# Kernel tuning notes

Measured on AMD Instinct MI355X. Metric: run time of the kernel, lower is better.

## Reference

```python
import jax, jax.numpy as jnp
import numpy as np

B, S, D, H = 4, 2048, 1024, 16
DK = D // H
EPS = 1e-5


def setup_inputs() -> dict:
    key = jax.random.key(0)
    ks = jax.random.split(key, 9)
    lim = 1.0 / np.sqrt(DK)  # nn.Linear default init range
    def u(k, shape):
        return jax.random.uniform(k, shape, jnp.float32, -lim, lim)
    return {
        "x": jax.random.normal(ks[0], (B, S, D), jnp.float32),
        "Wq": u(ks[1], (H, DK, DK)),
        "bq": u(ks[2], (H, DK)),
        "Wk": u(ks[3], (H, DK, DK)),
        "bk": u(ks[4], (H, DK)),
        "Wv": u(ks[5], (H, DK, DK)),
        "bv": u(ks[6], (H, DK)),
        "gamma": jnp.ones((D,), jnp.float32),
        "beta": jnp.zeros((D,), jnp.float32),
    }


def reference(x, Wq, bq, Wk, bk, Wv, bv, gamma, beta):
    b, s, d = x.shape
    h, dk = Wq.shape[0], Wq.shape[1]
    xh = x.reshape(b, s, h, dk)  # chunk along feature dim -> per-head slices
    # per-head linear projections (heads batched into one einsum)
    Q = jnp.einsum("bshd,hde->bshe", xh, Wq) + bq
    K = jnp.einsum("bshd,hde->bshe", xh, Wk) + bk
    V = jnp.einsum("bshd,hde->bshe", xh, Wv) + bv
    scale = jnp.sqrt(jnp.asarray(dk, x.dtype))
    scores = jnp.einsum("bshe,bthe->bhst", Q, K) / scale  # [B,H,S,S]
    causal = jnp.tril(jnp.ones((s, s), bool))  # apply_mask=True
    scores = jnp.where(causal, scores, -jnp.inf)
    P = jax.nn.softmax(scores, axis=-1)
    O = jnp.einsum("bhst,bthe->bshe", P, V).reshape(b, s, d)  # concat heads
    # dropout is identity in eval mode; residual + LayerNorm
    y = O + x
    mu = jnp.mean(y, axis=-1, keepdims=True)
    var = jnp.mean(jnp.square(y - mu), axis=-1, keepdims=True)
    return (y - mu) * jax.lax.rsqrt(var + EPS) * gamma + beta
```

## Files before the change

kernel.cpp:

```cpp
#include <hip/hip_runtime.h>
#include <hip/hip_bf16.h>

typedef __bf16 bf16_t;
typedef bf16_t bf16x8 __attribute__((ext_vector_type(8)));
typedef bf16_t bf16x4 __attribute__((ext_vector_type(4)));
typedef float f32x4 __attribute__((ext_vector_type(4)));

#define SEQ    2048
#define DHEAD  64
#define DMODEL 1024
#define KVB    64
#define BHN    64

__device__ __forceinline__ f32x4 mfma16(bf16x8 a, bf16x8 b, f32x4 c) {
  return __builtin_amdgcn_mfma_f32_16x16x32_bf16(a, b, c, 0, 0, 0);
}

__device__ __forceinline__ void gload16(void* l, const void* g) {
  __builtin_amdgcn_global_load_lds(
      (const __attribute__((address_space(1))) unsigned int*)g,
      (__attribute__((address_space(3))) unsigned int*)l,
      16, 0, 0);
}

__global__ __launch_bounds__(256) void qkv_kernel(
    const float* __restrict__ x,
    const float* __restrict__ Wq, const float* __restrict__ bq,
    const float* __restrict__ Wk, const float* __restrict__ bk,
    const float* __restrict__ Wv, const float* __restrict__ bv,
    bf16_t* __restrict__ Qw, bf16_t* __restrict__ Kw, bf16_t* __restrict__ VTw) {
  __shared__ __align__(16) char x_lds[256 * 128];
  __shared__ __align__(16) char w_lds[8192];

  const int bh = blockIdx.y;
  const int b = bh >> 4, h = bh & 15;
  const int s0 = blockIdx.x * 256;
  const int t = threadIdx.x;
  const int w = t >> 6, lane = t & 63;
  const int lo = lane & 15, g = lane >> 4;

#pragma unroll
  for (int p = 0; p < 8; ++p) {
    const int row = p * 32 + (t >> 3);
    const int c = t & 7;
    const float* xp = x + ((size_t)(b * SEQ + s0 + row)) * DMODEL + h * DHEAD + c * 8;
    const float4 f0 = *(const float4*)xp;
    const float4 f1 = *(const float4*)(xp + 4);
    bf16x8 v;
    v[0] = (bf16_t)f0.x; v[1] = (bf16_t)f0.y; v[2] = (bf16_t)f0.z; v[3] = (bf16_t)f0.w;
    v[4] = (bf16_t)f1.x; v[5] = (bf16_t)f1.y; v[6] = (bf16_t)f1.z; v[7] = (bf16_t)f1.w;
    *(bf16x8*)(x_lds + row * 128 + ((c * 16) ^ ((row & 7) << 4))) = v;
  }
  __syncthreads();

  for (int wi = 0; wi < 3; ++wi) {
    const float* Wp = (wi == 0) ? Wq : (wi == 1) ? Wk : Wv;
    const float* Bp = (wi == 0) ? bq : (wi == 1) ? bk : bv;
    bf16_t* Op      = (wi == 0) ? Qw : Kw;

    if (wi > 0) __syncthreads();
    {
      const int d = t >> 2, e0 = (t & 3) * 16;
      const float* wp = Wp + (size_t)(h * 64 + d) * 64 + e0;
      const float4 f0 = *(const float4*)(wp);
      const float4 f1 = *(const float4*)(wp + 4);
      const float4 f2 = *(const float4*)(wp + 8);
      const float4 f3 = *(const float4*)(wp + 12);
      float vals[16];
      vals[0] = f0.x; vals[1] = f0.y; vals[2] = f0.z; vals[3] = f0.w;
      vals[4] = f1.x; vals[5] = f1.y; vals[6] = f1.z; vals[7] = f1.w;
      vals[8] = f2.x; vals[9] = f2.y; vals[10] = f2.z; vals[11] = f2.w;
      vals[12] = f3.x; vals[13] = f3.y; vals[14] = f3.z; vals[15] = f3.w;
#pragma unroll
      for (int j = 0; j < 16; ++j) {
        const int e = e0 + j;
        *(bf16_t*)(w_lds + e * 128 + ((2 * d) ^ ((e & 7) << 4))) = (bf16_t)vals[j];
      }
    }
    __syncthreads();

    bf16x8 wf[2][4];
    float bias[4];
#pragma unroll
    for (int ct = 0; ct < 4; ++ct) {
      bias[ct] = Bp[h * 64 + ct * 16 + lo];
#pragma unroll
      for (int ks = 0; ks < 2; ++ks)
        wf[ks][ct] = *(const bf16x8*)(w_lds + (ct * 16 + lo) * 128 +
                                      ((ks * 64 + g * 16) ^ ((lo & 7) << 4)));
    }
    if (wi == 2) __syncthreads();

    const float sc = (wi == 0) ? 0.125f : 1.0f;
#pragma unroll
    for (int it = 0; it < 4; ++it) {
      const int r0 = it * 64 + w * 16;
      bf16x8 xa[2];
#pragma unroll
      for (int ks = 0; ks < 2; ++ks) {
        const int row = r0 + lo;
        xa[ks] = *(const bf16x8*)(x_lds + row * 128 +
                                  ((ks * 64 + g * 16) ^ ((row & 7) << 4)));
      }
      f32x4 acc[4];
#pragma unroll
      for (int ct = 0; ct < 4; ++ct) {
        f32x4 a = (f32x4){0.f, 0.f, 0.f, 0.f};
        a = mfma16(xa[0], wf[0][ct], a);
        a = mfma16(xa[1], wf[1][ct], a);
        acc[ct] = a;
      }
      if (wi < 2) {
#pragma unroll
        for (int ct = 0; ct < 4; ++ct)
#pragma unroll
          for (int r = 0; r < 4; ++r) {
            const int srow = s0 + r0 + g * 4 + r;
            Op[((size_t)bh * SEQ + srow) * DHEAD + ct * 16 + lo] =
                (bf16_t)((acc[ct][r] + bias[ct]) * sc);
          }
      } else {
#pragma unroll
        for (int ct = 0; ct < 4; ++ct) {
          bf16x4 pk;
#pragma unroll
          for (int r = 0; r < 4; ++r) pk[r] = (bf16_t)(acc[ct][r] + bias[ct]);
          *(bf16x4*)(w_lds + (ct * 16 + lo) * 128 +
                     ((w * 32 + g * 8) ^ ((lo & 7) << 4))) = pk;
        }
        __syncthreads();
        {
          const int e = t >> 2, c4 = t & 3;
          const int sw = (e & 7) << 4;
          const bf16x8 v0 = *(const bf16x8*)(w_lds + e * 128 + ((c4 * 32) ^ sw));
          const bf16x8 v1 = *(const bf16x8*)(w_lds + e * 128 + ((c4 * 32 + 16) ^ sw));
          bf16_t* vp = VTw + ((size_t)bh * DHEAD + e) * SEQ + s0 + it * 64 + c4 * 16;
          *(bf16x8*)(vp) = v0;
          *(bf16x8*)(vp + 8) = v1;
        }
        __syncthreads();
      }
    }
  }
}

__global__ __launch_bounds__(256) void attn_kernel(
    const bf16_t* __restrict__ Qw, const bf16_t* __restrict__ Kw,
    const bf16_t* __restrict__ VTw, float* __restrict__ Out) {
  __shared__ __align__(16) char stage_lds[2][16384];
  __shared__ __align__(16) char p_lds[4][4096];

  const int f = blockIdx.x;
  const int bh = (f & 7) * 8 + ((f >> 3) & 7);
  const int pair = f >> 6;
  const int b = bh >> 4, h = bh & 15;

  const int t = threadIdx.x;
  const int w = t >> 6, lane = t & 63;
  const int lo = lane & 15, g = lane >> 4;
  char* pbase = &p_lds[w][0];

  const int strow = w * 8 + (lane >> 3);
  const int scol = ((lane & 7) * 16) ^ ((lane >> 3) << 4);
  const char* Kbase = (const char*)(Kw + (size_t)bh * SEQ * DHEAD);
  const char* Vbase = (const char*)(VTw + (size_t)bh * DHEAD * SEQ);
  const bf16_t* Qb = Qw + (size_t)bh * SEQ * DHEAD;

  for (int half = 0; half < 2; ++half) {
    const int qt = half ? (15 - pair) : pair;
    const int q0 = qt * 128;
    const int kts = 2 * qt + 2;

    bf16x8 qf[2][2];
#pragma unroll
    for (int s = 0; s < 2; ++s) {
      const bf16_t* qp = Qb + (size_t)(q0 + w * 32 + s * 16 + lo) * DHEAD + g * 8;
      qf[s][0] = *(const bf16x8*)(qp);
      qf[s][1] = *(const bf16x8*)(qp + 32);
    }
    float m_run[2] = {-1e30f, -1e30f};
    float l_run[2] = {0.f, 0.f};
    f32x4 oacc[2][4];
#pragma unroll
    for (int s = 0; s < 2; ++s)
#pragma unroll
      for (int dt = 0; dt < 4; ++dt) oacc[s][dt] = (f32x4){0.f, 0.f, 0.f, 0.f};

    __syncthreads();
    {
      char* db = &stage_lds[0][0];
#pragma unroll
      for (int p = 0; p < 2; ++p) {
        gload16(db + p * 4096 + w * 1024,
                Kbase + (size_t)(p * 32 + strow) * 128 + scol);
        gload16(db + 8192 + p * 4096 + w * 1024,
                Vbase + (size_t)(p * 32 + strow) * 4096 + scol);
      }
    }
    int cur = 0;
    for (int kt = 0; kt < kts; ++kt) {
      const int kv0 = kt * KVB;
      __syncthreads();
      if (kt + 1 < kts) {
        const int nk = kv0 + KVB;
        char* db = &stage_lds[cur ^ 1][0];
#pragma unroll
        for (int p = 0; p < 2; ++p) {
          gload16(db + p * 4096 + w * 1024,
                  Kbase + (size_t)(nk + p * 32 + strow) * 128 + scol);
          gload16(db + 8192 + p * 4096 + w * 1024,
                  Vbase + (size_t)(p * 32 + strow) * 4096 + (size_t)nk * 2 + scol);
        }
      }
      const char* kb = &stage_lds[cur][0];
      const char* vb = kb + 8192;

      bf16x8 kf[2][4];
#pragma unroll
      for (int ks = 0; ks < 2; ++ks)
#pragma unroll
        for (int ct = 0; ct < 4; ++ct)
          kf[ks][ct] = *(const bf16x8*)(kb + (ct * 16 + lo) * 128 +
                                        ((ks * 64 + g * 16) ^ ((lo & 7) << 4)));
      f32x4 sa[2][4];
#pragma unroll
      for (int s = 0; s < 2; ++s) {
        const int qs0 = q0 + w * 32 + s * 16;
        if (kv0 > qs0 + 15) continue;
#pragma unroll
        for (int ct = 0; ct < 4; ++ct) {
          f32x4 a = (f32x4){0.f, 0.f, 0.f, 0.f};
          a = mfma16(kf[0][ct], qf[s][0], a);
          a = mfma16(kf[1][ct], qf[s][1], a);
          sa[s][ct] = a;
        }
      }
#pragma unroll
      for (int s = 0; s < 2; ++s) {
        const int qs0 = q0 + w * 32 + s * 16;
        if (kv0 > qs0 + 15) continue;
        const int q = qs0 + lo;
        if (kv0 + 63 > qs0) {
#pragma unroll
          for (int ct = 0; ct < 4; ++ct)
#pragma unroll
            for (int r = 0; r < 4; ++r) {
              const int kv = kv0 + ct * 16 + g * 4 + r;
              if (kv > q) sa[s][ct][r] = -1e30f;
            }
        }
        float mt = -1e30f;
#pragma unroll
        for (int ct = 0; ct < 4; ++ct)
          mt = fmaxf(mt, fmaxf(fmaxf(sa[s][ct][0], sa[s][ct][1]),
                               fmaxf(sa[s][ct][2], sa[s][ct][3])));
        mt = fmaxf(mt, __shfl_xor(mt, 16));
        mt = fmaxf(mt, __shfl_xor(mt, 32));
        if (__any(mt > m_run[s] + 8.f)) {
          const float mn = fmaxf(m_run[s], mt);
          const float rs = __expf(m_run[s] - mn);
          l_run[s] *= rs;
          m_run[s] = mn;
#pragma unroll
          for (int r = 0; r < 4; ++r) {
            const float fr = __shfl(rs, g * 4 + r);
#pragma unroll
            for (int dt = 0; dt < 4; ++dt) oacc[s][dt][r] *= fr;
          }
        }
        float lt = 0.f;
        const float m = m_run[s];
#pragma unroll
        for (int ct = 0; ct < 4; ++ct) {
          bf16x4 pk;
#pragma unroll
          for (int r = 0; r < 4; ++r) {
            const float pv = __expf(sa[s][ct][r] - m);
            lt += pv;
            pk[r] = (bf16_t)pv;
          }
          *(bf16x4*)(pbase + (s * 16 + lo) * 128 +
                     ((ct * 32 + g * 8) ^ ((lo & 7) << 4))) = pk;
        }
        lt += __shfl_xor(lt, 16);
        lt += __shfl_xor(lt, 32);
        l_run[s] += lt;
      }
      bf16x8 vf[2][4];
#pragma unroll
      for (int ks = 0; ks < 2; ++ks)
#pragma unroll
        for (int dt = 0; dt < 4; ++dt)
          vf[ks][dt] = *(const bf16x8*)(vb + (dt * 16 + lo) * 128 +
                                        ((ks * 64 + g * 16) ^ ((lo & 7) << 4)));
#pragma unroll
      for (int s = 0; s < 2; ++s) {
        const int qs0 = q0 + w * 32 + s * 16;
        if (kv0 > qs0 + 15) continue;
#pragma unroll
        for (int ks = 0; ks < 2; ++ks) {
          const bf16x8 pa = *(const bf16x8*)(pbase + (s * 16 + lo) * 128 +
                                             ((ks * 64 + g * 16) ^ ((lo & 7) << 4)));
#pragma unroll
          for (int dt = 0; dt < 4; ++dt)
            oacc[s][dt] = mfma16(pa, vf[ks][dt], oacc[s][dt]);
        }
      }
      cur ^= 1;
    }
#pragma unroll
    for (int s = 0; s < 2; ++s) {
      const float inv = 1.f / l_run[s];
#pragma unroll
      for (int r = 0; r < 4; ++r) {
        const float fr = __shfl(inv, g * 4 + r);
        const int srow = q0 + w * 32 + s * 16 + g * 4 + r;
        float* op = Out + ((size_t)b * SEQ + srow) * DMODEL + h * DHEAD;
#pragma unroll
        for (int dt = 0; dt < 4; ++dt) op[dt * 16 + lo] = oacc[s][dt][r] * fr;
      }
    }
  }
}

__global__ __launch_bounds__(256) void ln_kernel(
    const float* __restrict__ x, const float* __restrict__ gamma,
    const float* __restrict__ beta, float* __restrict__ out) {
  __shared__ float red[8];
  const int row = blockIdx.x;
  const int t = threadIdx.x;
  float* orow = out + (size_t)row * DMODEL;
  const float* xrow = x + (size_t)row * DMODEL;

  const float4 o = *(const float4*)(orow + t * 4);
  const float4 xv = *(const float4*)(xrow + t * 4);
  float y0 = o.x + xv.x, y1 = o.y + xv.y, y2 = o.z + xv.z, y3 = o.w + xv.w;
  float s = y0 + y1 + y2 + y3;
  float sq = y0 * y0 + y1 * y1 + y2 * y2 + y3 * y3;
#pragma unroll
  for (int m = 1; m < 64; m <<= 1) {
    s += __shfl_xor(s, m);
    sq += __shfl_xor(sq, m);
  }
  const int w = t >> 6;
  if ((t & 63) == 0) { red[w] = s; red[4 + w] = sq; }
  __syncthreads();
  const float S = red[0] + red[1] + red[2] + red[3];
  const float SQ = red[4] + red[5] + red[6] + red[7];
  const float mu = S * (1.f / DMODEL);
  const float var = SQ * (1.f / DMODEL) - mu * mu;
  const float rstd = rsqrtf(var + 1e-5f);
  const float4 gv = *(const float4*)(gamma + t * 4);
  const float4 bv = *(const float4*)(beta + t * 4);
  float4 res;
  res.x = (y0 - mu) * rstd * gv.x + bv.x;
  res.y = (y1 - mu) * rstd * gv.y + bv.y;
  res.z = (y2 - mu) * rstd * gv.z + bv.z;
  res.w = (y3 - mu) * rstd * gv.w + bv.w;
  *(float4*)(orow + t * 4) = res;
}

extern "C" void kernel_launch(void* const* d_in, const int* in_sizes, int n_in,
                              void* d_out, int out_size, void* d_ws, size_t ws_size,
                              hipStream_t stream) {
  const float* x     = (const float*)d_in[0];
  const float* Wq    = (const float*)d_in[1];
  const float* bq    = (const float*)d_in[2];
  const float* Wk    = (const float*)d_in[3];
  const float* bk    = (const float*)d_in[4];
  const float* Wv    = (const float*)d_in[5];
  const float* bv    = (const float*)d_in[6];
  const float* gamma = (const float*)d_in[7];
  const float* beta  = (const float*)d_in[8];
  float* out = (float*)d_out;

  const size_t per = (size_t)BHN * SEQ * DHEAD;
  bf16_t* Qw  = (bf16_t*)d_ws;
  bf16_t* Kw  = Qw + per;
  bf16_t* VTw = Kw + per;

  qkv_kernel<<<dim3(8, 64), 256, 0, stream>>>(x, Wq, bq, Wk, bk, Wv, bv, Qw, Kw, VTw);
  attn_kernel<<<dim3(512), 256, 0, stream>>>(Qw, Kw, VTw, out);
  ln_kernel<<<dim3(8192), 256, 0, stream>>>(x, gamma, beta, out);
}
```

Before: 197.4 us.

## Shrink attention query tile to 64, use exp2 softmax, simplify QKV stores

The attention kernel now processes 64-row query tiles with one 16-row slice per wave, launching twice as many blocks and halving the P scratch buffer, with occupancy hinted via launch bounds. Softmax uses exp2 with log2e folded into the Q scale, and MFMA sections are wrapped with s_setprio. The QKV kernel computes Q/K transposed so it can store vectorized bf16x4, and it writes V transposed directly to global memory instead of staging through LDS with extra barriers. The aim is better load balance, occupancy and cheaper exponentials, at the cost of less K/V reuse per block and more global K/V traffic.

```diff
diff --git a/kernel.cpp b/kernel.cpp
--- a/kernel.cpp
+++ b/kernel.cpp
@@ -11,6 +11,7 @@
 #define DMODEL 1024
 #define KVB    64
 #define BHN    64
+#define LOG2E  1.4426950408889634f
 
 __device__ __forceinline__ f32x4 mfma16(bf16x8 a, bf16x8 b, f32x4 c) {
   return __builtin_amdgcn_mfma_f32_16x16x32_bf16(a, b, c, 0, 0, 0);
@@ -80,18 +81,24 @@
     __syncthreads();
 
     bf16x8 wf[2][4];
-    float bias[4];
-#pragma unroll
-    for (int ct = 0; ct < 4; ++ct) {
-      bias[ct] = Bp[h * 64 + ct * 16 + lo];
+#pragma unroll
+    for (int ct = 0; ct < 4; ++ct)
 #pragma unroll
       for (int ks = 0; ks < 2; ++ks)
         wf[ks][ct] = *(const bf16x8*)(w_lds + (ct * 16 + lo) * 128 +
                                       ((ks * 64 + g * 16) ^ ((lo & 7) << 4)));
-    }
-    if (wi == 2) __syncthreads();
-
-    const float sc = (wi == 0) ? 0.125f : 1.0f;
+    float4 biasv[4];
+    float biass[4];
+    if (wi < 2) {
+#pragma unroll
+      for (int ct = 0; ct < 4; ++ct)
+        biasv[ct] = *(const float4*)(Bp + h * 64 + ct * 16 + g * 4);
+    } else {
+#pragma unroll
+      for (int ct = 0; ct < 4; ++ct) biass[ct] = Bp[h * 64 + ct * 16 + lo];
+    }
+
+    const float sc = (wi == 0) ? (0.125f * LOG2E) : 1.0f;
 #pragma unroll
     for (int it = 0; it < 4; ++it) {
       const int r0 = it * 64 + w * 16;
@@ -102,53 +109,39 @@
         xa[ks] = *(const bf16x8*)(x_lds + row * 128 +
                                   ((ks * 64 + g * 16) ^ ((row & 7) << 4)));
       }
-      f32x4 acc[4];
-#pragma unroll
-      for (int ct = 0; ct < 4; ++ct) {
-        f32x4 a = (f32x4){0.f, 0.f, 0.f, 0.f};
-        a = mfma16(xa[0], wf[0][ct], a);
-        a = mfma16(xa[1], wf[1][ct], a);
-        acc[ct] = a;
-      }
       if (wi < 2) {
 #pragma unroll
-        for (int ct = 0; ct < 4; ++ct)
-#pragma unroll
-          for (int r = 0; r < 4; ++r) {
-            const int srow = s0 + r0 + g * 4 + r;
-            Op[((size_t)bh * SEQ + srow) * DHEAD + ct * 16 + lo] =
-                (bf16_t)((acc[ct][r] + bias[ct]) * sc);
-          }
+        for (int ct = 0; ct < 4; ++ct) {
+          f32x4 a = (f32x4){0.f, 0.f, 0.f, 0.f};
+          a = mfma16(wf[0][ct], xa[0], a);
+          a = mfma16(wf[1][ct], xa[1], a);
+          bf16x4 pk;
+#pragma unroll
+          for (int r = 0; r < 4; ++r)
+            pk[r] = (bf16_t)((a[r] + ((const float*)&biasv[ct])[r]) * sc);
+          *(bf16x4*)(Op + ((size_t)bh * SEQ + s0 + r0 + lo) * DHEAD + ct * 16 + g * 4) = pk;
+        }
       } else {
 #pragma unroll
         for (int ct = 0; ct < 4; ++ct) {
+          f32x4 a = (f32x4){0.f, 0.f, 0.f, 0.f};
+          a = mfma16(xa[0], wf[0][ct], a);
+          a = mfma16(xa[1], wf[1][ct], a);
           bf16x4 pk;
 #pragma unroll
-          for (int r = 0; r < 4; ++r) pk[r] = (bf16_t)(acc[ct][r] + bias[ct]);
-          *(bf16x4*)(w_lds + (ct * 16 + lo) * 128 +
-                     ((w * 32 + g * 8) ^ ((lo & 7) << 4))) = pk;
-        }
-        __syncthreads();
-        {
-          const int e = t >> 2, c4 = t & 3;
-          const int sw = (e & 7) << 4;
-          const bf16x8 v0 = *(const bf16x8*)(w_lds + e * 128 + ((c4 * 32) ^ sw));
-          const bf16x8 v1 = *(const bf16x8*)(w_lds + e * 128 + ((c4 * 32 + 16) ^ sw));
-          bf16_t* vp = VTw + ((size_t)bh * DHEAD + e) * SEQ + s0 + it * 64 + c4 * 16;
-          *(bf16x8*)(vp) = v0;
-          *(bf16x8*)(vp + 8) = v1;
-        }
-        __syncthreads();
+          for (int r = 0; r < 4; ++r) pk[r] = (bf16_t)(a[r] + biass[ct]);
+          *(bf16x4*)(VTw + ((size_t)bh * DHEAD + ct * 16 + lo) * SEQ + s0 + r0 + g * 4) = pk;
+        }
       }
     }
   }
 }
 
-__global__ __launch_bounds__(256) void attn_kernel(
+__global__ __launch_bounds__(256, 4) void attn_kernel(
     const bf16_t* __restrict__ Qw, const bf16_t* __restrict__ Kw,
     const bf16_t* __restrict__ VTw, float* __restrict__ Out) {
   __shared__ __align__(16) char stage_lds[2][16384];
-  __shared__ __align__(16) char p_lds[4][4096];
+  __shared__ __align__(16) char p_lds[4][2048];
 
   const int f = blockIdx.x;
   const int bh = (f & 7) * 8 + ((f >> 3) & 7);
@@ -165,26 +158,24 @@
   const char* Kbase = (const char*)(Kw + (size_t)bh * SEQ * DHEAD);
   const char* Vbase = (const char*)(VTw + (size_t)bh * DHEAD * SEQ);
   const bf16_t* Qb = Qw + (size_t)bh * SEQ * DHEAD;
+  const int swz = (lo & 7) << 4;
 
   for (int half = 0; half < 2; ++half) {
-    const int qt = half ? (15 - pair) : pair;
-    const int q0 = qt * 128;
-    const int kts = 2 * qt + 2;
-
-    bf16x8 qf[2][2];
-#pragma unroll
-    for (int s = 0; s < 2; ++s) {
-      const bf16_t* qp = Qb + (size_t)(q0 + w * 32 + s * 16 + lo) * DHEAD + g * 8;
-      qf[s][0] = *(const bf16x8*)(qp);
-      qf[s][1] = *(const bf16x8*)(qp + 32);
-    }
-    float m_run[2] = {-1e30f, -1e30f};
-    float l_run[2] = {0.f, 0.f};
-    f32x4 oacc[2][4];
-#pragma unroll
-    for (int s = 0; s < 2; ++s)
-#pragma unroll
-      for (int dt = 0; dt < 4; ++dt) oacc[s][dt] = (f32x4){0.f, 0.f, 0.f, 0.f};
+    const int qt = half ? (31 - pair) : pair;
+    const int q0 = qt * 64;
+    const int qw0 = q0 + w * 16;
+    const int kts = qt + 1;
+
+    bf16x8 qf[2];
+    {
+      const bf16_t* qp = Qb + (size_t)(qw0 + lo) * DHEAD + g * 8;
+      qf[0] = *(const bf16x8*)(qp);
+      qf[1] = *(const bf16x8*)(qp + 32);
+    }
+    float m_run = -1e30f, l_run = 0.f;
+    f32x4 oacc[4];
+#pragma unroll
+    for (int dt = 0; dt < 4; ++dt) oacc[dt] = (f32x4){0.f, 0.f, 0.f, 0.f};
 
     __syncthreads();
     {
@@ -221,104 +212,89 @@
 #pragma unroll
         for (int ct = 0; ct < 4; ++ct)
           kf[ks][ct] = *(const bf16x8*)(kb + (ct * 16 + lo) * 128 +
-                                        ((ks * 64 + g * 16) ^ ((lo & 7) << 4)));
-      f32x4 sa[2][4];
-#pragma unroll
-      for (int s = 0; s < 2; ++s) {
-        const int qs0 = q0 + w * 32 + s * 16;
-        if (kv0 > qs0 + 15) continue;
-#pragma unroll
-        for (int ct = 0; ct < 4; ++ct) {
-          f32x4 a = (f32x4){0.f, 0.f, 0.f, 0.f};
-          a = mfma16(kf[0][ct], qf[s][0], a);
-          a = mfma16(kf[1][ct], qf[s][1], a);
-          sa[s][ct] = a;
-        }
-      }
-#pragma unroll
-      for (int s = 0; s < 2; ++s) {
-        const int qs0 = q0 + w * 32 + s * 16;
-        if (kv0 > qs0 + 15) continue;
-        const int q = qs0 + lo;
-        if (kv0 + 63 > qs0) {
-#pragma unroll
-          for (int ct = 0; ct < 4; ++ct)
-#pragma unroll
-            for (int r = 0; r < 4; ++r) {
-              const int kv = kv0 + ct * 16 + g * 4 + r;
-              if (kv > q) sa[s][ct][r] = -1e30f;
-            }
-        }
-        float mt = -1e30f;
+                                        ((ks * 64 + g * 16) ^ swz));
+      f32x4 sa[4];
+      __builtin_amdgcn_s_setprio(1);
+#pragma unroll
+      for (int ct = 0; ct < 4; ++ct) {
+        f32x4 a = (f32x4){0.f, 0.f, 0.f, 0.f};
+        a = mfma16(kf[0][ct], qf[0], a);
+        a = mfma16(kf[1][ct], qf[1], a);
+        sa[ct] = a;
+      }
+      __builtin_amdgcn_s_setprio(0);
+
+      if (kt == qt) {
+        const int q = qw0 + lo;
 #pragma unroll
         for (int ct = 0; ct < 4; ++ct)
-          mt = fmaxf(mt, fmaxf(fmaxf(sa[s][ct][0], sa[s][ct][1]),
-                               fmaxf(sa[s][ct][2], sa[s][ct][3])));
-        mt = fmaxf(mt, __shfl_xor(mt, 16));
-        mt = fmaxf(mt, __shfl_xor(mt, 32));
-        if (__any(mt > m_run[s] + 8.f)) {
-          const float mn = fmaxf(m_run[s], mt);
-          const float rs = __expf(m_run[s] - mn);
-          l_run[s] *= rs;
-          m_run[s] = mn;
 #pragma unroll
           for (int r = 0; r < 4; ++r) {
-            const float fr = __shfl(rs, g * 4 + r);
-#pragma unroll
-            for (int dt = 0; dt < 4; ++dt) oacc[s][dt][r] *= fr;
+            const int kv = kv0 + ct * 16 + g * 4 + r;
+            if (kv > q) sa[ct][r] = -1e30f;
           }
-        }
-        float lt = 0.f;
-        const float m = m_run[s];
-#pragma unroll
-        for (int ct = 0; ct < 4; ++ct) {
-          bf16x4 pk;
-#pragma unroll
-          for (int r = 0; r < 4; ++r) {
-            const float pv = __expf(sa[s][ct][r] - m);
-            lt += pv;
-            pk[r] = (bf16_t)pv;
-          }
-          *(bf16x4*)(pbase + (s * 16 + lo) * 128 +
-                     ((ct * 32 + g * 8) ^ ((lo & 7) << 4))) = pk;
-        }
-        lt += __shfl_xor(lt, 16);
-        lt += __shfl_xor(lt, 32);
-        l_run[s] += lt;
-      }
+      }
+      float mt = -1e30f;
+#pragma unroll
+      for (int ct = 0; ct < 4; ++ct)
+        mt = fmaxf(mt, fmaxf(fmaxf(sa[ct][0], sa[ct][1]),
+                             fmaxf(sa[ct][2], sa[ct][3])));
+      mt = fmaxf(mt, __shfl_xor(mt, 16));
+      mt = fmaxf(mt, __shfl_xor(mt, 32));
+      if (__any(mt > m_run + 8.f)) {
+        const float mn = fmaxf(m_run, mt);
+        const float rs = exp2f(m_run - mn);
+        l_run *= rs;
+        m_run = mn;
+#pragma unroll
+        for (int r = 0; r < 4; ++r) {
+          const float fr = __shfl(rs, g * 4 + r);
+#pragma unroll
+          for (int dt = 0; dt < 4; ++dt) oacc[dt][r] *= fr;
+        }
+      }
+      float lt = 0.f;
+#pragma unroll
+      for (int ct = 0; ct < 4; ++ct) {
+        bf16x4 pk;
+#pragma unroll
+        for (int r = 0; r < 4; ++r) {
+          const float pv = exp2f(sa[ct][r] - m_run);
+          lt += pv;
+          pk[r] = (bf16_t)pv;
+        }
+        *(bf16x4*)(pbase + lo * 128 + ((ct * 32 + g * 8) ^ swz)) = pk;
+      }
+      lt += __shfl_xor(lt, 16);
+      lt += __shfl_xor(lt, 32);
+      l_run += lt;
+
       bf16x8 vf[2][4];
 #pragma unroll
       for (int ks = 0; ks < 2; ++ks)
 #pragma unroll
         for (int dt = 0; dt < 4; ++dt)
           vf[ks][dt] = *(const bf16x8*)(vb + (dt * 16 + lo) * 128 +
-                                        ((ks * 64 + g * 16) ^ ((lo & 7) << 4)));
-#pragma unroll
-      for (int s = 0; s < 2; ++s) {
-        const int qs0 = q0 + w * 32 + s * 16;
-        if (kv0 > qs0 + 15) continue;
-#pragma unroll
-        for (int ks = 0; ks < 2; ++ks) {
-          const bf16x8 pa = *(const bf16x8*)(pbase + (s * 16 + lo) * 128 +
-                                             ((ks * 64 + g * 16) ^ ((lo & 7) << 4)));
-#pragma unroll
-          for (int dt = 0; dt < 4; ++dt)
-            oacc[s][dt] = mfma16(pa, vf[ks][dt], oacc[s][dt]);
-        }
-      }
+                                        ((ks * 64 + g * 16) ^ swz));
+      __builtin_amdgcn_s_setprio(1);
+#pragma unroll
+      for (int ks = 0; ks < 2; ++ks) {
+        const bf16x8 pa = *(const bf16x8*)(pbase + lo * 128 + ((ks * 64 + g * 16) ^ swz));
+#pragma unroll
+        for (int dt = 0; dt < 4; ++dt)
+          oacc[dt] = mfma16(pa, vf[ks][dt], oacc[dt]);
+      }
+      __builtin_amdgcn_s_setprio(0);
       cur ^= 1;
     }
-#pragma unroll
-    for (int s = 0; s < 2; ++s) {
-      const float inv = 1.f / l_run[s];
-#pragma unroll
-      for (int r = 0; r < 4; ++r) {
-        const float fr = __shfl(inv, g * 4 + r);
-        const int srow = q0 + w * 32 + s * 16 + g * 4 + r;
-        float* op = Out + ((size_t)b * SEQ + srow) * DMODEL + h * DHEAD;
-#pragma unroll
-        for (int dt = 0; dt < 4; ++dt) op[dt * 16 + lo] = oacc[s][dt][r] * fr;
-      }
+    const float inv = 1.f / l_run;
+#pragma unroll
+    for (int r = 0; r < 4; ++r) {
+      const float fr = __shfl(inv, g * 4 + r);
+      const int srow = qw0 + g * 4 + r;
+      float* op = Out + ((size_t)b * SEQ + srow) * DMODEL + h * DHEAD;
+#pragma unroll
+      for (int dt = 0; dt < 4; ++dt) op[dt * 16 + lo] = oacc[dt][r] * fr;
     }
   }
 }
@@ -380,6 +356,6 @@
   bf16_t* VTw = Kw + per;
 
   qkv_kernel<<<dim3(8, 64), 256, 0, stream>>>(x, Wq, bq, Wk, bk, Wv, bv, Qw, Kw, VTw);
-  attn_kernel<<<dim3(512), 256, 0, stream>>>(Qw, Kw, VTw, out);
+  attn_kernel<<<dim3(1024), 256, 0, stream>>>(Qw, Kw, VTw, out);
   ln_kernel<<<dim3(8192), 256, 0, stream>>>(x, gamma, beta, out);
 }
```

After: 198.9 us. About the same (+0.8%).
